# Optimization experiments

Hardware: AMD Instinct MI355X
Metric: run time of the kernel (lower is better)

## Reference

```python
import jax, jax.numpy as jnp
import numpy as np

B, T, E, H, V = 32, 120, 300, 256, 32000
C, G = 512, 7

def setup_inputs() -> dict:
    key = jax.random.key(0)
    ks = jax.random.split(key, 8)
    s = lambda k, shape, sc: (jax.random.normal(k, shape, jnp.float32) * sc)
    return {
        "features": jax.random.normal(ks[0], (B, C, G, G), jnp.float32),
        "embeddings": jax.random.normal(ks[1], (B, T, E), jnp.float32),
        "W_init": s(ks[2], (H, C), 0.04),          # nn.Linear(512, num_layers*H)
        "b_init": jnp.zeros((H,), jnp.float32),
        "W_fc2": s(ks[3], (H, C * G * G), 0.006),   # nn.Linear(512*49, H)
        "b_fc2": jnp.zeros((H,), jnp.float32),
        "W_ih": s(ks[4], (3 * H, E + H), 0.04),     # GRU weight_ih_l0 (r,z,n rows)
        "b_ih": jnp.zeros((3 * H,), jnp.float32),
        "W_hh": s(ks[5], (3 * H, H), 0.06),         # GRU weight_hh_l0
        "b_hh": jnp.zeros((3 * H,), jnp.float32),
        "W_fc": s(ks[6], (V, H), 0.06),             # nn.Linear(H, vocab)
        "b_fc": jnp.zeros((V,), jnp.float32),
        "length": T,
    }

def reference(features, embeddings, W_init, b_init, W_fc2, b_fc2,
              W_ih, b_ih, W_hh, b_hh, W_fc, b_fc, length):
    Bq, Cq = features.shape[0], features.shape[1]
    Hq = W_hh.shape[1]
    # init_hidden_state: [B,C,7,7] -> [B,49,C]
    f = jnp.transpose(features, (0, 2, 3, 1)).reshape(Bq, -1, Cq)
    h0 = f.mean(axis=1) @ W_init.T + b_init                      # [B,H], num_layers=1
    # flatten + fc2, broadcast over time, concat with embeddings
    feat = f.reshape(Bq, -1) @ W_fc2.T + b_fc2                   # [B,H]
    x = jnp.concatenate(
        [embeddings,
         jnp.broadcast_to(feat[:, None, :], (Bq, embeddings.shape[1], Hq))],
        axis=-1)                                                  # [B,T,E+H]
    xs = jnp.transpose(x[:, :length], (1, 0, 2))                  # [T,B,E+H]
    # precompute input-side gate projections for all timesteps (one big GEMM)
    gi = jnp.einsum('tbi,gi->tbg', xs, W_ih) + b_ih               # [T,B,3H]
    def step(h, g_x):
        g_h = h @ W_hh.T + b_hh
        r = jax.nn.sigmoid(g_x[..., :Hq] + g_h[..., :Hq])
        z = jax.nn.sigmoid(g_x[..., Hq:2 * Hq] + g_h[..., Hq:2 * Hq])
        n = jnp.tanh(g_x[..., 2 * Hq:] + r * g_h[..., 2 * Hq:])
        h_new = (1.0 - z) * n + z * h
        return h_new, h_new
    _, hs = jax.lax.scan(step, h0, gi)                            # [T,B,H]
    # per-step fc (dropout p=0.3 is identity in eval mode)
    logits = jnp.einsum('tbh,vh->btv', hs, W_fc) + b_fc           # [B,T,V]
    return logits
```

## Files before the change

kernel.cpp:

```cpp
#include <hip/hip_runtime.h>
#include <hip/hip_bf16.h>

#define BB 32
#define TT 120
#define EE 300
#define HH 256
#define VV 32000
#define CC 512
#define GG 49
#define KIN 556
#define CF 25088

typedef __attribute__((ext_vector_type(8))) short bf16x8;
typedef __attribute__((ext_vector_type(4))) float f32x4;

__device__ __forceinline__ float bpair_lo(unsigned int u) { return __uint_as_float(u << 16); }
__device__ __forceinline__ float bpair_hi(unsigned int u) { return __uint_as_float(u & 0xFFFF0000u); }

__device__ __forceinline__ unsigned int packbf(float a, float b) {
    union { __hip_bfloat16 h; unsigned short u; } ua, ub;
    ua.h = __float2bfloat16(a); ub.h = __float2bfloat16(b);
    return (unsigned int)ua.u | ((unsigned int)ub.u << 16);
}

#if defined(__has_builtin)
#  if __has_builtin(__builtin_amdgcn_fdot2_f32_bf16)
#    define USE_DOT2 1
#  endif
#endif
#ifndef USE_DOT2
#  define USE_DOT2 0
#endif

#if USE_DOT2
typedef __bf16 bf2_t __attribute__((ext_vector_type(2)));
__device__ __forceinline__ float dot2bf(unsigned int w, unsigned int h, float c) {
    return __builtin_amdgcn_fdot2_f32_bf16(__builtin_bit_cast(bf2_t, w),
                                           __builtin_bit_cast(bf2_t, h), c, false);
}
#else
__device__ __forceinline__ float dot2bf(unsigned int w, unsigned int h, float c) {
    c = fmaf(bpair_lo(w), bpair_lo(h), c);
    c = fmaf(bpair_hi(w), bpair_hi(h), c);
    return c;
}
#endif

__global__ void __launch_bounds__(256) k_h0(const float* __restrict__ features,
                                            const float* __restrict__ W_init,
                                            const float* __restrict__ b_init,
                                            float* __restrict__ h0) {
    int b  = blockIdx.x;
    int hc = blockIdx.y;
    __shared__ float mf[CC];
    __shared__ float red[8][33];
    {
        const float* p = features + (size_t)b * CF + (size_t)threadIdx.x * 2 * GG;
        float s0 = 0.f, s1 = 0.f;
#pragma unroll
        for (int i = 0; i < GG; ++i) s0 += p[i];
#pragma unroll
        for (int i = 0; i < GG; ++i) s1 += p[GG + i];
        mf[threadIdx.x * 2]     = s0 * (1.0f / 49.0f);
        mf[threadIdx.x * 2 + 1] = s1 * (1.0f / 49.0f);
    }
    __syncthreads();
    int h  = threadIdx.x & 31;
    int kg = threadIdx.x >> 5;
    int gh = hc * 32 + h;
    const float* w = W_init + (size_t)gh * CC + kg * 64;
    const float* m = mf + kg * 64;
    float s = 0.f;
#pragma unroll
    for (int k = 0; k < 64; k += 4) {
        float4 w4 = *(const float4*)(w + k);
        s += m[k] * w4.x + m[k + 1] * w4.y + m[k + 2] * w4.z + m[k + 3] * w4.w;
    }
    red[kg][h] = s;
    __syncthreads();
    if (threadIdx.x < 32) {
        float t = b_init[hc * 32 + threadIdx.x];
#pragma unroll
        for (int g = 0; g < 8; ++g) t += red[g][threadIdx.x];
        h0[b * HH + hc * 32 + threadIdx.x] = t;
    }
}

__global__ void __launch_bounds__(256) k_cvthh(const float* __restrict__ W_hh,
                                               unsigned int* __restrict__ whh_bf) {
    int idx = blockIdx.x * 256 + threadIdx.x;
    float2 w2 = *(const float2*)(W_hh + (size_t)idx * 2);
    whh_bf[idx] = packbf(w2.x, w2.y);
}

__global__ void __launch_bounds__(256) k_fc2a(const float* __restrict__ features,
                                              const float* __restrict__ W_fc2,
                                              float* __restrict__ part) {
    int kc = blockIdx.x;
    __shared__ float xs[98][BB];
    for (int idx = threadIdx.x; idx < 98 * BB; idx += 256) {
        int ii = idx >> 5, b = idx & 31;
        int ig = kc * 98 + ii;
        int c = ig & 511, p = ig >> 9;
        xs[ii][b] = features[(size_t)b * CF + c * GG + p];
    }
    __syncthreads();
    int h = threadIdx.x;
    float acc[BB];
#pragma unroll
    for (int b = 0; b < BB; ++b) acc[b] = 0.f;
    const float* wp = W_fc2 + (size_t)h * CF + kc * 98;
    for (int ii = 0; ii < 98; ii += 2) {
        float2 w2 = *(const float2*)(wp + ii);
        const float4* x0 = (const float4*)&xs[ii][0];
        const float4* x1 = (const float4*)&xs[ii + 1][0];
#pragma unroll
        for (int q = 0; q < 8; ++q) {
            float4 a4 = x0[q], b4 = x1[q];
            acc[4 * q + 0] += w2.x * a4.x + w2.y * b4.x;
            acc[4 * q + 1] += w2.x * a4.y + w2.y * b4.y;
            acc[4 * q + 2] += w2.x * a4.z + w2.y * b4.z;
            acc[4 * q + 3] += w2.x * a4.w + w2.y * b4.w;
        }
    }
    float* pp = part + (size_t)kc * (BB * 256) + h;
#pragma unroll
    for (int b = 0; b < BB; ++b) pp[b * 256] = acc[b];
}

__global__ void __launch_bounds__(256) k_fc2b(const float* __restrict__ part,
                                              const float* __restrict__ b_fc2,
                                              float* __restrict__ feat) {
    int b  = blockIdx.x;
    int hc = blockIdx.y;
    int h  = threadIdx.x & 31;
    int kg = threadIdx.x >> 5;
    int gh = hc * 32 + h;
    __shared__ float red[8][33];
    const float* pp = part + (size_t)kg * 32 * (BB * 256) + b * 256 + gh;
    float s = 0.f;
#pragma unroll
    for (int kc = 0; kc < 32; ++kc) s += pp[(size_t)kc * (BB * 256)];
    red[kg][h] = s;
    __syncthreads();
    if (threadIdx.x < 32) {
        float t = b_fc2[hc * 32 + threadIdx.x];
#pragma unroll
        for (int g = 0; g < 8; ++g) t += red[g][threadIdx.x];
        feat[b * HH + hc * 32 + threadIdx.x] = t;
    }
}

__global__ void __launch_bounds__(256) k_gi(const float* __restrict__ emb,
                                            const float* __restrict__ feat,
                                            const float* __restrict__ W_ih,
                                            const float* __restrict__ b_ih,
                                            float* __restrict__ gi) {
    __shared__ float As[64][68];
    __shared__ float Bs[64][68];
    int n0 = blockIdx.x * 64;
    int m0 = blockIdx.y * 64;
    int tid = threadIdx.x;
    int tm = (tid & 15) * 4;
    int tn = (tid >> 4) * 4;
    float acc[4][4] = {};

    for (int kc = 0; kc < 9; ++kc) {
        int k0 = kc * 64;
        __syncthreads();
#pragma unroll
        for (int s = 0; s < 4; ++s) {
            int slot = tid * 4 + s;
            int mr = slot >> 4;
            int kl = (slot & 15) * 4;
            int m = m0 + mr;
            int t = m >> 5, b = m & 31;
            int kg = k0 + kl;
            float4 v;
            if (kg + 4 <= EE) {
                v = *(const float4*)(emb + ((size_t)b * TT + t) * EE + kg);
            } else if (kg >= EE && kg + 4 <= KIN) {
                v = *(const float4*)(feat + (size_t)b * HH + (kg - EE));
            } else {
                float tmp[4];
#pragma unroll
                for (int q = 0; q < 4; ++q) {
                    int kq = kg + q;
                    tmp[q] = (kq < EE) ? emb[((size_t)b * TT + t) * EE + kq]
                           : (kq < KIN) ? feat[(size_t)b * HH + (kq - EE)] : 0.f;
                }
                v = *(float4*)tmp;
            }
            As[kl + 0][mr] = v.x;
            As[kl + 1][mr] = v.y;
            As[kl + 2][mr] = v.z;
            As[kl + 3][mr] = v.w;
        }
#pragma unroll
        for (int s = 0; s < 4; ++s) {
            int slot = tid * 4 + s;
            int nr = slot >> 4;
            int kl = (slot & 15) * 4;
            int kg = k0 + kl;
            int gidx = n0 + nr;
            float4 v;
            if (kg + 4 <= KIN) {
                v = *(const float4*)(W_ih + (size_t)gidx * KIN + kg);
            } else {
                float tmp[4];
#pragma unroll
                for (int q = 0; q < 4; ++q) {
                    int kq = kg + q;
                    tmp[q] = (kq < KIN) ? W_ih[(size_t)gidx * KIN + kq] : 0.f;
                }
                v = *(float4*)tmp;
            }
            Bs[kl + 0][nr] = v.x;
            Bs[kl + 1][nr] = v.y;
            Bs[kl + 2][nr] = v.z;
            Bs[kl + 3][nr] = v.w;
        }
        __syncthreads();
        int kmax = (kc == 8) ? 44 : 64;
        for (int k = 0; k < kmax; ++k) {
            float4 av = *(const float4*)&As[k][tm];
            float4 bv = *(const float4*)&Bs[k][tn];
            const float* ap = (const float*)&av;
            const float* bp = (const float*)&bv;
#pragma unroll
            for (int i = 0; i < 4; ++i)
#pragma unroll
                for (int j = 0; j < 4; ++j)
                    acc[i][j] = fmaf(ap[i], bp[j], acc[i][j]);
        }
    }
    float4 bias = *(const float4*)(b_ih + n0 + tn);
    const float* bp = (const float*)&bias;
#pragma unroll
    for (int i = 0; i < 4; ++i) {
        int m = m0 + tm + i;
        float4 o;
        o.x = acc[i][0] + bp[0];
        o.y = acc[i][1] + bp[1];
        o.z = acc[i][2] + bp[2];
        o.w = acc[i][3] + bp[3];
        *(float4*)(gi + (size_t)m * 768 + n0 + tn) = o;
    }
}

__device__ __forceinline__ void gru_body(int b, const float* __restrict__ h0,
                                         const float* __restrict__ gi,
                                         const unsigned int* __restrict__ whh_bf,
                                         const float* __restrict__ b_hh,
                                         __hip_bfloat16* __restrict__ hA,
                                         unsigned int* h_pk, float* hf,
                                         float* r_sh, float* z_sh) {
    int jp = threadIdx.x;
    int j  = jp & 255;
    int g  = jp >> 8;
    const unsigned int* wr = whh_bf + (size_t)jp * 128;
    float bias = b_hh[jp];
    if (jp < HH) hf[jp] = h0[b * HH + jp];
    __syncthreads();
    if (jp < 128) h_pk[jp] = packbf(hf[2 * jp], hf[2 * jp + 1]);
    __syncthreads();

    for (int t = 0; t < TT; ++t) {
        float a0 = 0.f, a1 = 0.f, a2 = 0.f, a3 = 0.f;
#pragma unroll
        for (int kk = 0; kk < 128; kk += 4) {
            uint4 wq = *(const uint4*)(wr + kk);
            uint4 hq = *(const uint4*)&h_pk[kk];
            a0 = dot2bf(wq.x, hq.x, a0);
            a1 = dot2bf(wq.y, hq.y, a1);
            a2 = dot2bf(wq.z, hq.z, a2);
            a3 = dot2bf(wq.w, hq.w, a3);
        }
        float a = (a0 + a1) + (a2 + a3);
        float gx = gi[((size_t)t * BB + b) * 768 + jp];
        if (g == 0)      r_sh[j] = 1.f / (1.f + __expf(-(gx + a + bias)));
        else if (g == 1) z_sh[j] = 1.f / (1.f + __expf(-(gx + a + bias)));
        __syncthreads();
        if (g == 2) {
            float n  = tanhf(gx + r_sh[j] * (a + bias));
            float z  = z_sh[j];
            float hn = (1.f - z) * n + z * hf[j];
            hf[j] = hn;
            hA[((size_t)b * TT + t) * HH + j] = __float2bfloat16(hn);
        }
        __syncthreads();
        if (jp < 128) h_pk[jp] = packbf(hf[2 * jp], hf[2 * jp + 1]);
        __syncthreads();
    }
}

__global__ void __launch_bounds__(768, 3) k_gru(const float* __restrict__ h0,
                                                const float* __restrict__ gi,
                                                const unsigned int* __restrict__ whh_bf,
                                                const float* __restrict__ b_hh,
                                                __hip_bfloat16* __restrict__ hA) {
    __shared__ unsigned int h_pk[128];
    __shared__ float hf[256];
    __shared__ float r_sh[256];
    __shared__ float z_sh[256];
    gru_body(blockIdx.x, h0, gi, whh_bf, b_hh, hA, h_pk, hf, r_sh, z_sh);
}

#define CVT_N4 2048000
__global__ void __launch_bounds__(768, 3) k_gru_cvt(const float* __restrict__ h0,
                                                    const float* __restrict__ gi,
                                                    const unsigned int* __restrict__ whh_bf,
                                                    const float* __restrict__ b_hh,
                                                    __hip_bfloat16* __restrict__ hA,
                                                    const float* __restrict__ W_fc,
                                                    __hip_bfloat16* __restrict__ wfc) {
    if (blockIdx.x >= 32) {
        size_t base = (size_t)(blockIdx.x - 32) * (768 * 4) + threadIdx.x;
#pragma unroll
        for (int q = 0; q < 4; ++q) {
            size_t fi = base + (size_t)q * 768;
            if (fi < CVT_N4) {
                float4 v = *((const float4*)W_fc + fi);
                __hip_bfloat16 o[4];
                o[0] = __float2bfloat16(v.x);
                o[1] = __float2bfloat16(v.y);
                o[2] = __float2bfloat16(v.z);
                o[3] = __float2bfloat16(v.w);
                *((uint2*)wfc + fi) = *(uint2*)o;
            }
        }
        return;
    }
    __shared__ unsigned int h_pk[128];
    __shared__ float hf[256];
    __shared__ float r_sh[256];
    __shared__ float z_sh[256];
    gru_body(blockIdx.x, h0, gi, whh_bf, b_hh, hA, h_pk, hf, r_sh, z_sh);
}

__global__ void k_cvt(const float* __restrict__ src, __hip_bfloat16* __restrict__ dst) {
    size_t i = ((size_t)blockIdx.x * 256 + threadIdx.x) * 4;
    float4 v = *(const float4*)(src + i);
    __hip_bfloat16 o[4];
    o[0] = __float2bfloat16(v.x);
    o[1] = __float2bfloat16(v.y);
    o[2] = __float2bfloat16(v.z);
    o[3] = __float2bfloat16(v.w);
    *(uint2*)(dst + i) = *(uint2*)o;
}

__global__ void __launch_bounds__(256) k_logits(const __hip_bfloat16* __restrict__ hA,
                                                const __hip_bfloat16* __restrict__ wfc,
                                                const float* __restrict__ b_fc,
                                                float* __restrict__ out) {
    __shared__ __align__(16) short smemAB[2][128][64];
    char* AsB = (char*)smemAB[0];
    char* BsB = (char*)smemAB[1];
    float* eb = (float*)smemAB;

    int nt = blockIdx.x;
    int mt = blockIdx.y;
    int tid  = threadIdx.x;
    int wave = tid >> 6, lane = tid & 63;
    int wm = wave >> 1, wn = wave & 1;
    int lr = lane & 15;
    int lk = lane >> 4;

    int rs = tid >> 3;
    int cs = tid & 7;
    const short* Ag = (const short*)hA  + (size_t)mt * 128 * HH + (size_t)rs * HH + cs * 8;
    const short* Bg = (const short*)wfc + (size_t)nt * 128 * HH + (size_t)rs * HH + cs * 8;
    int wswz = (cs ^ (rs & 7)) * 16;
    int wofs[4];
#pragma unroll
    for (int p = 0; p < 4; ++p) wofs[p] = (p * 32 + rs) * 128 + wswz;

    f32x4 acc[4][4] = {};

#define LOADT(kt, GA, GB)                                                        \
    do {                                                                         \
        _Pragma("unroll") for (int p = 0; p < 4; ++p)                            \
            GA[p] = *(const bf16x8*)(Ag + (size_t)p * 32 * HH + (kt) * 64);      \
        _Pragma("unroll") for (int p = 0; p < 4; ++p)                            \
            GB[p] = *(const bf16x8*)(Bg + (size_t)p * 32 * HH + (kt) * 64);      \
    } while (0)

#define STORET(GA, GB)                                                           \
    do {                                                                         \
        _Pragma("unroll") for (int p = 0; p < 4; ++p)                            \
            *(bf16x8*)(AsB + wofs[p]) = GA[p];                                   \
        _Pragma("unroll") for (int p = 0; p < 4; ++p)                            \
            *(bf16x8*)(BsB + wofs[p]) = GB[p];                                   \
    } while (0)

#define COMPUTE()                                                                \
    do {                                                                         \
        _Pragma("unroll") for (int kk = 0; kk < 2; ++kk) {                       \
            bf16x8 af[4], bg[4];                                                 \
            _Pragma("unroll") for (int i = 0; i < 4; ++i) {                      \
                int r = wm * 64 + i * 16 + lr;                                   \
                af[i] = *(const bf16x8*)(AsB + r * 128 + (((kk * 4 + lk) ^ (r & 7)) * 16)); \
            }                                                                    \
            _Pragma("unroll") for (int j = 0; j < 4; ++j) {                      \
                int r = wn * 64 + j * 16 + lr;                                   \
                bg[j] = *(const bf16x8*)(BsB + r * 128 + (((kk * 4 + lk) ^ (r & 7)) * 16)); \
            }                                                                    \
            _Pragma("unroll") for (int i = 0; i < 4; ++i)                        \
                _Pragma("unroll") for (int j = 0; j < 4; ++j)                    \
                    acc[i][j] = __builtin_amdgcn_mfma_f32_16x16x32_bf16(af[i], bg[j], acc[i][j], 0, 0, 0); \
        }                                                                        \
    } while (0)

    bf16x8 gA[4], gB[4], gA2[4], gB2[4];
    LOADT(0, gA, gB);
    STORET(gA, gB);   LOADT(1, gA2, gB2); __syncthreads(); COMPUTE(); __syncthreads();
    STORET(gA2, gB2); LOADT(2, gA, gB);   __syncthreads(); COMPUTE(); __syncthreads();
    STORET(gA, gB);   LOADT(3, gA2, gB2); __syncthreads(); COMPUTE(); __syncthreads();
    STORET(gA2, gB2);                     __syncthreads(); COMPUTE();

#undef LOADT
#undef STORET
#undef COMPUTE

    int mloc = wm * 64;
#pragma unroll 1
    for (int nh = 0; nh < 2; ++nh) {
        __syncthreads();
        if (wn == nh) {
#pragma unroll
            for (int j = 0; j < 4; ++j) {
                int v = nt * 128 + nh * 64 + j * 16 + lr;
                float bias = b_fc[v];
#pragma unroll
                for (int i = 0; i < 4; ++i) {
#pragma unroll
                    for (int q = 0; q < 4; ++q)
                        eb[(mloc + i * 16 + lk * 4 + q) * 64 + j * 16 + lr] = acc[i][j][q] + bias;
                }
            }
        }
        __syncthreads();
        size_t obase = (size_t)(mt * 128) * VV + nt * 128 + nh * 64;
#pragma unroll
        for (int pass = 0; pass < 8; ++pass) {
            int idx = pass * 256 + tid;
            int row = idx >> 4;
            int c4 = (idx & 15) * 4;
            float4 vv = *(const float4*)&eb[row * 64 + c4];
            *(float4*)(out + obase + (size_t)row * VV + c4) = vv;
        }
    }
}

extern "C" void kernel_launch(void* const* d_in, const int* in_sizes, int n_in,
                              void* d_out, int out_size, void* d_ws, size_t ws_size,
                              hipStream_t stream) {
    (void)in_sizes; (void)n_in; (void)out_size;
    const float* features   = (const float*)d_in[0];
    const float* embeddings = (const float*)d_in[1];
    const float* W_init     = (const float*)d_in[2];
    const float* b_init     = (const float*)d_in[3];
    const float* W_fc2      = (const float*)d_in[4];
    const float* b_fc2      = (const float*)d_in[5];
    const float* W_ih       = (const float*)d_in[6];
    const float* b_ih       = (const float*)d_in[7];
    const float* W_hh       = (const float*)d_in[8];
    const float* b_hh       = (const float*)d_in[9];
    const float* W_fc       = (const float*)d_in[10];
    const float* b_fc       = (const float*)d_in[11];

    char* ws = (char*)d_ws;
    float* feat   = (float*)(ws + 65536);
    float* hbuf0  = (float*)(ws + 98304);
    __hip_bfloat16* hA = (__hip_bfloat16*)(ws + 131072);
    float* gi     = (float*)(ws + 2097152);
    float* part   = (float*)(ws + 2097152);
    unsigned int* whh_bf = (unsigned int*)(ws + 13893632);
    float* outp = (float*)d_out;

    int fused = (ws_size >= 30670848u);
    __hip_bfloat16* wfc = fused ? (__hip_bfloat16*)(ws + 14286848)
                                : (__hip_bfloat16*)(ws + 2097152);

    k_h0<<<dim3(32, 8), 256, 0, stream>>>(features, W_init, b_init, hbuf0);
    k_cvthh<<<384, 256, 0, stream>>>(W_hh, whh_bf);
    k_fc2a<<<256, 256, 0, stream>>>(features, W_fc2, part);
    k_fc2b<<<dim3(32, 8), 256, 0, stream>>>(part, b_fc2, feat);
    k_gi<<<dim3(12, 60), 256, 0, stream>>>(embeddings, feat, W_ih, b_ih, gi);
    if (fused) {
        k_gru_cvt<<<32 + 667, 768, 0, stream>>>(hbuf0, gi, whh_bf, b_hh, hA, W_fc, wfc);
    } else {
        k_gru<<<32, 768, 0, stream>>>(hbuf0, gi, whh_bf, b_hh, hA);
        k_cvt<<<8000, 256, 0, stream>>>(W_fc, wfc);
    }
    k_logits<<<dim3(250, 30), 256, 0, stream>>>(hA, wfc, b_fc, outp);
}
```

Baseline: 436.8 us.

## Merge preprocessing kernels and register-prefetch next tile in gi GEMM

Merges the three independent setup kernels (h0 projection, W_hh bf16 conversion, fc2 partial GEMM) into one launch that picks a role from the block index. This removes two kernel launches and lets the three jobs share the GPU at once. The gi GEMM now loads the next K-tile into registers while the current tile is being computed, so global load latency overlaps with FMAs. In exchange the merged kernel's shared memory is the union of all three roles, and the prefetch uses more registers.

```diff
diff --git a/kernel.cpp b/kernel.cpp
--- a/kernel.cpp
+++ b/kernel.cpp
@@ -46,86 +46,87 @@
 }
 #endif
 
-__global__ void __launch_bounds__(256) k_h0(const float* __restrict__ features,
-                                            const float* __restrict__ W_init,
-                                            const float* __restrict__ b_init,
-                                            float* __restrict__ h0) {
-    int b  = blockIdx.x;
-    int hc = blockIdx.y;
+__global__ void __launch_bounds__(256) k_pre(const float* __restrict__ features,
+                                             const float* __restrict__ W_fc2,
+                                             float* __restrict__ part,
+                                             const float* __restrict__ W_hh,
+                                             unsigned int* __restrict__ whh_bf,
+                                             const float* __restrict__ W_init,
+                                             const float* __restrict__ b_init,
+                                             float* __restrict__ h0) {
+    __shared__ float xs[98][BB];
     __shared__ float mf[CC];
     __shared__ float red[8][33];
-    {
-        const float* p = features + (size_t)b * CF + (size_t)threadIdx.x * 2 * GG;
-        float s0 = 0.f, s1 = 0.f;
-#pragma unroll
-        for (int i = 0; i < GG; ++i) s0 += p[i];
-#pragma unroll
-        for (int i = 0; i < GG; ++i) s1 += p[GG + i];
-        mf[threadIdx.x * 2]     = s0 * (1.0f / 49.0f);
-        mf[threadIdx.x * 2 + 1] = s1 * (1.0f / 49.0f);
-    }
-    __syncthreads();
-    int h  = threadIdx.x & 31;
-    int kg = threadIdx.x >> 5;
-    int gh = hc * 32 + h;
-    const float* w = W_init + (size_t)gh * CC + kg * 64;
-    const float* m = mf + kg * 64;
-    float s = 0.f;
-#pragma unroll
-    for (int k = 0; k < 64; k += 4) {
-        float4 w4 = *(const float4*)(w + k);
-        s += m[k] * w4.x + m[k + 1] * w4.y + m[k + 2] * w4.z + m[k + 3] * w4.w;
-    }
-    red[kg][h] = s;
-    __syncthreads();
-    if (threadIdx.x < 32) {
-        float t = b_init[hc * 32 + threadIdx.x];
-#pragma unroll
-        for (int g = 0; g < 8; ++g) t += red[g][threadIdx.x];
-        h0[b * HH + hc * 32 + threadIdx.x] = t;
-    }
-}
-
-__global__ void __launch_bounds__(256) k_cvthh(const float* __restrict__ W_hh,
-                                               unsigned int* __restrict__ whh_bf) {
-    int idx = blockIdx.x * 256 + threadIdx.x;
-    float2 w2 = *(const float2*)(W_hh + (size_t)idx * 2);
-    whh_bf[idx] = packbf(w2.x, w2.y);
-}
-
-__global__ void __launch_bounds__(256) k_fc2a(const float* __restrict__ features,
-                                              const float* __restrict__ W_fc2,
-                                              float* __restrict__ part) {
-    int kc = blockIdx.x;
-    __shared__ float xs[98][BB];
-    for (int idx = threadIdx.x; idx < 98 * BB; idx += 256) {
-        int ii = idx >> 5, b = idx & 31;
-        int ig = kc * 98 + ii;
-        int c = ig & 511, p = ig >> 9;
-        xs[ii][b] = features[(size_t)b * CF + c * GG + p];
-    }
-    __syncthreads();
-    int h = threadIdx.x;
-    float acc[BB];
-#pragma unroll
-    for (int b = 0; b < BB; ++b) acc[b] = 0.f;
-    const float* wp = W_fc2 + (size_t)h * CF + kc * 98;
-    for (int ii = 0; ii < 98; ii += 2) {
-        float2 w2 = *(const float2*)(wp + ii);
-        const float4* x0 = (const float4*)&xs[ii][0];
-        const float4* x1 = (const float4*)&xs[ii + 1][0];
-#pragma unroll
-        for (int q = 0; q < 8; ++q) {
-            float4 a4 = x0[q], b4 = x1[q];
-            acc[4 * q + 0] += w2.x * a4.x + w2.y * b4.x;
-            acc[4 * q + 1] += w2.x * a4.y + w2.y * b4.y;
-            acc[4 * q + 2] += w2.x * a4.z + w2.y * b4.z;
-            acc[4 * q + 3] += w2.x * a4.w + w2.y * b4.w;
-        }
-    }
-    float* pp = part + (size_t)kc * (BB * 256) + h;
-#pragma unroll
-    for (int b = 0; b < BB; ++b) pp[b * 256] = acc[b];
+    int bid = blockIdx.x;
+    if (bid < 256) {
+        int kc = bid;
+        for (int idx = threadIdx.x; idx < 98 * BB; idx += 256) {
+            int ii = idx >> 5, b = idx & 31;
+            int ig = kc * 98 + ii;
+            int c = ig & 511, p = ig >> 9;
+            xs[ii][b] = features[(size_t)b * CF + c * GG + p];
+        }
+        __syncthreads();
+        int h = threadIdx.x;
+        float acc[BB];
+#pragma unroll
+        for (int b = 0; b < BB; ++b) acc[b] = 0.f;
+        const float* wp = W_fc2 + (size_t)h * CF + kc * 98;
+        for (int ii = 0; ii < 98; ii += 2) {
+            float2 w2 = *(const float2*)(wp + ii);
+            const float4* x0 = (const float4*)&xs[ii][0];
+            const float4* x1 = (const float4*)&xs[ii + 1][0];
+#pragma unroll
+            for (int q = 0; q < 8; ++q) {
+                float4 a4 = x0[q], b4 = x1[q];
+                acc[4 * q + 0] += w2.x * a4.x + w2.y * b4.x;
+                acc[4 * q + 1] += w2.x * a4.y + w2.y * b4.y;
+                acc[4 * q + 2] += w2.x * a4.z + w2.y * b4.z;
+                acc[4 * q + 3] += w2.x * a4.w + w2.y * b4.w;
+            }
+        }
+        float* pp = part + (size_t)kc * (BB * 256) + h;
+#pragma unroll
+        for (int b = 0; b < BB; ++b) pp[b * 256] = acc[b];
+    } else if (bid < 640) {
+        int idx = (bid - 256) * 256 + threadIdx.x;
+        float2 w2 = *(const float2*)(W_hh + (size_t)idx * 2);
+        whh_bf[idx] = packbf(w2.x, w2.y);
+    } else {
+        int lb = bid - 640;
+        int b  = lb >> 3;
+        int hc = lb & 7;
+        {
+            const float* p = features + (size_t)b * CF + (size_t)threadIdx.x * 2 * GG;
+            float s0 = 0.f, s1 = 0.f;
+#pragma unroll
+            for (int i = 0; i < GG; ++i) s0 += p[i];
+#pragma unroll
+            for (int i = 0; i < GG; ++i) s1 += p[GG + i];
+            mf[threadIdx.x * 2]     = s0 * (1.0f / 49.0f);
+            mf[threadIdx.x * 2 + 1] = s1 * (1.0f / 49.0f);
+        }
+        __syncthreads();
+        int h  = threadIdx.x & 31;
+        int kg = threadIdx.x >> 5;
+        int gh = hc * 32 + h;
+        const float* w = W_init + (size_t)gh * CC + kg * 64;
+        const float* m = mf + kg * 64;
+        float s = 0.f;
+#pragma unroll
+        for (int k = 0; k < 64; k += 4) {
+            float4 w4 = *(const float4*)(w + k);
+            s += m[k] * w4.x + m[k + 1] * w4.y + m[k + 2] * w4.z + m[k + 3] * w4.w;
+        }
+        red[kg][h] = s;
+        __syncthreads();
+        if (threadIdx.x < 32) {
+            float t = b_init[hc * 32 + threadIdx.x];
+#pragma unroll
+            for (int g = 0; g < 8; ++g) t += red[g][threadIdx.x];
+            h0[b * HH + hc * 32 + threadIdx.x] = t;
+        }
+    }
 }
 
 __global__ void __launch_bounds__(256) k_fc2b(const float* __restrict__ part,
@@ -165,61 +166,73 @@
     int tn = (tid >> 4) * 4;
     float acc[4][4] = {};
 
+    int mrA[4], klA[4];
+#pragma unroll
+    for (int s = 0; s < 4; ++s) {
+        int slot = tid * 4 + s;
+        mrA[s] = slot >> 4;
+        klA[s] = (slot & 15) * 4;
+    }
+
+    float4 ra[4], rb[4];
+
+#define LOADG(KC)                                                                 \
+    do {                                                                          \
+        int k0_ = (KC) * 64;                                                      \
+        _Pragma("unroll") for (int s = 0; s < 4; ++s) {                           \
+            int m = m0 + mrA[s];                                                  \
+            int t = m >> 5, b = m & 31;                                           \
+            int kg = k0_ + klA[s];                                                \
+            if (kg + 4 <= EE) {                                                   \
+                ra[s] = *(const float4*)(emb + ((size_t)b * TT + t) * EE + kg);   \
+            } else if (kg >= EE && kg + 4 <= KIN) {                               \
+                ra[s] = *(const float4*)(feat + (size_t)b * HH + (kg - EE));      \
+            } else {                                                              \
+                float tmp[4];                                                     \
+                _Pragma("unroll") for (int q = 0; q < 4; ++q) {                   \
+                    int kq = kg + q;                                              \
+                    tmp[q] = (kq < EE) ? emb[((size_t)b * TT + t) * EE + kq]      \
+                           : (kq < KIN) ? feat[(size_t)b * HH + (kq - EE)] : 0.f; \
+                }                                                                 \
+                ra[s] = *(float4*)tmp;                                            \
+            }                                                                     \
+        }                                                                         \
+        _Pragma("unroll") for (int s = 0; s < 4; ++s) {                           \
+            int gidx = n0 + mrA[s];                                               \
+            int kg = k0_ + klA[s];                                                \
+            if (kg + 4 <= KIN) {                                                  \
+                rb[s] = *(const float4*)(W_ih + (size_t)gidx * KIN + kg);         \
+            } else {                                                              \
+                float tmp[4];                                                     \
+                _Pragma("unroll") for (int q = 0; q < 4; ++q) {                   \
+                    int kq = kg + q;                                              \
+                    tmp[q] = (kq < KIN) ? W_ih[(size_t)gidx * KIN + kq] : 0.f;    \
+                }                                                                 \
+                rb[s] = *(float4*)tmp;                                            \
+            }                                                                     \
+        }                                                                         \
+    } while (0)
+
+#define STORES()                                                                  \
+    do {                                                                          \
+        _Pragma("unroll") for (int s = 0; s < 4; ++s) {                           \
+            As[klA[s] + 0][mrA[s]] = ra[s].x;                                     \
+            As[klA[s] + 1][mrA[s]] = ra[s].y;                                     \
+            As[klA[s] + 2][mrA[s]] = ra[s].z;                                     \
+            As[klA[s] + 3][mrA[s]] = ra[s].w;                                     \
+            Bs[klA[s] + 0][mrA[s]] = rb[s].x;                                     \
+            Bs[klA[s] + 1][mrA[s]] = rb[s].y;                                     \
+            Bs[klA[s] + 2][mrA[s]] = rb[s].z;                                     \
+            Bs[klA[s] + 3][mrA[s]] = rb[s].w;                                     \
+        }                                                                         \
+    } while (0)
+
+    LOADG(0);
+#pragma unroll 1
     for (int kc = 0; kc < 9; ++kc) {
-        int k0 = kc * 64;
-        __syncthreads();
-#pragma unroll
-        for (int s = 0; s < 4; ++s) {
-            int slot = tid * 4 + s;
-            int mr = slot >> 4;
-            int kl = (slot & 15) * 4;
-            int m = m0 + mr;
-            int t = m >> 5, b = m & 31;
-            int kg = k0 + kl;
-            float4 v;
-            if (kg + 4 <= EE) {
-                v = *(const float4*)(emb + ((size_t)b * TT + t) * EE + kg);
-            } else if (kg >= EE && kg + 4 <= KIN) {
-                v = *(const float4*)(feat + (size_t)b * HH + (kg - EE));
-            } else {
-                float tmp[4];
-#pragma unroll
-                for (int q = 0; q < 4; ++q) {
-                    int kq = kg + q;
-                    tmp[q] = (kq < EE) ? emb[((size_t)b * TT + t) * EE + kq]
-                           : (kq < KIN) ? feat[(size_t)b * HH + (kq - EE)] : 0.f;
-                }
-                v = *(float4*)tmp;
-            }
-            As[kl + 0][mr] = v.x;
-            As[kl + 1][mr] = v.y;
-            As[kl + 2][mr] = v.z;
-            As[kl + 3][mr] = v.w;
-        }
-#pragma unroll
-        for (int s = 0; s < 4; ++s) {
-            int slot = tid * 4 + s;
-            int nr = slot >> 4;
-            int kl = (slot & 15) * 4;
-            int kg = k0 + kl;
-            int gidx = n0 + nr;
-            float4 v;
-            if (kg + 4 <= KIN) {
-                v = *(const float4*)(W_ih + (size_t)gidx * KIN + kg);
-            } else {
-                float tmp[4];
-#pragma unroll
-                for (int q = 0; q < 4; ++q) {
-                    int kq = kg + q;
-                    tmp[q] = (kq < KIN) ? W_ih[(size_t)gidx * KIN + kq] : 0.f;
-                }
-                v = *(float4*)tmp;
-            }
-            Bs[kl + 0][nr] = v.x;
-            Bs[kl + 1][nr] = v.y;
-            Bs[kl + 2][nr] = v.z;
-            Bs[kl + 3][nr] = v.w;
-        }
+        __syncthreads();
+        STORES();
+        if (kc < 8) LOADG(kc + 1);
         __syncthreads();
         int kmax = (kc == 8) ? 44 : 64;
         for (int k = 0; k < kmax; ++k) {
@@ -234,6 +247,9 @@
                     acc[i][j] = fmaf(ap[i], bp[j], acc[i][j]);
         }
     }
+#undef LOADG
+#undef STORES
+
     float4 bias = *(const float4*)(b_ih + n0 + tn);
     const float* bp = (const float*)&bias;
 #pragma unroll
@@ -482,9 +498,7 @@
     __hip_bfloat16* wfc = fused ? (__hip_bfloat16*)(ws + 14286848)
                                 : (__hip_bfloat16*)(ws + 2097152);
 
-    k_h0<<<dim3(32, 8), 256, 0, stream>>>(features, W_init, b_init, hbuf0);
-    k_cvthh<<<384, 256, 0, stream>>>(W_hh, whh_bf);
-    k_fc2a<<<256, 256, 0, stream>>>(features, W_fc2, part);
+    k_pre<<<896, 256, 0, stream>>>(features, W_fc2, part, W_hh, whh_bf, W_init, b_init, hbuf0);
     k_fc2b<<<dim3(32, 8), 256, 0, stream>>>(part, b_fc2, feat);
     k_gi<<<dim3(12, 60), 256, 0, stream>>>(embeddings, feat, W_ih, b_ih, gi);
     if (fused) {
```

Measured after the change: 431.0 us. No clear change (-1.3%).
